# Optimization experiments

Hardware: AMD Instinct MI355X
Metric: run time of the kernel (lower is better)

Reference implementation:

```python
import jax, jax.numpy as jnp
import numpy as np

N = 27            # hardcoded node count in the module
D = 1024          # state_dim
E = D * 5         # MHA embed dim = 5120
H = 4             # n_heads


def setup_inputs() -> dict:
    key = jax.random.key(0)
    ks = jax.random.split(key, 6)
    s = 0.02
    return {
        "node_states": jax.random.normal(ks[0], (N, D, 5), jnp.float32),
        "hist_prev": jax.random.normal(ks[1], (N, D, 5), jnp.float32),
        "granger_w": jax.random.normal(ks[2], (1, 2 * E), jnp.float32) * s,
        "granger_b": jnp.zeros((1,), jnp.float32),
        "in_proj_w": jax.random.normal(ks[3], (3 * E, E), jnp.float32) * s,
        "in_proj_b": jnp.zeros((3 * E,), jnp.float32),
        "out_proj_w": jax.random.normal(ks[4], (E, E), jnp.float32) * s,
        "out_proj_b": jnp.zeros((E,), jnp.float32),
        "light_hertz": 500,
    }


def _mha(x, in_w, in_b, out_w, out_b):
    # x: [N, E]; torch MultiheadAttention with q=k=v=x, batch of 1
    qkv = x @ in_w.T + in_b                       # [N, 3E]
    q, k, v = jnp.split(qkv, 3, axis=-1)          # each [N, E]
    hd = E // H
    q = q.reshape(N, H, hd).transpose(1, 0, 2)    # [H, N, hd]
    k = k.reshape(N, H, hd).transpose(1, 0, 2)
    v = v.reshape(N, H, hd).transpose(1, 0, 2)
    scores = jnp.einsum('hqd,hkd->hqk', q, k) / jnp.sqrt(jnp.float32(hd))
    attn = jax.nn.softmax(scores, axis=-1)        # [H, N, N]
    o = jnp.einsum('hqk,hkd->hqd', attn, v)       # [H, N, hd]
    o = o.transpose(1, 0, 2).reshape(N, E)
    return o @ out_w.T + out_b                    # [N, E]


def reference(node_states, hist_prev, granger_w, granger_b,
              in_proj_w, in_proj_b, out_proj_w, out_proj_b, light_hertz):
    node_flat = node_states.reshape(N, E)         # [N, E]
    hist_flat = hist_prev.reshape(N, E)           # [N, E]

    # Granger pairwise test, vectorized: pred_input = [hist[j], node[i]]
    # score[i, j] = sigmoid(hist[j] . w_h + node[i] . w_n + b)
    w_h = granger_w[0, :E]
    w_n = granger_w[0, E:]
    col = node_flat @ w_n                          # [N] -> varies with i
    row = hist_flat @ w_h                          # [N] -> varies with j
    adj = jax.nn.sigmoid(col[:, None] + row[None, :] + granger_b[0])  # [N, N]
    causal_adj = adj * (1.0 - jnp.eye(N, dtype=adj.dtype))            # zero diagonal

    hertz_weight = jnp.clip(jnp.float32(light_hertz) / 1000.0, 0.1, 1.0)
    attended = _mha(node_flat, in_proj_w, in_proj_b, out_proj_w, out_proj_b)
    out = (attended * hertz_weight).reshape(N, D, 5)
    return out, causal_adj
```

## Files before the change

kernel.cpp:

```cpp
#include <hip/hip_runtime.h>

#define NROW 27
#define EDIM 5120
#define QKVDIM 15360
#define HD 1280

typedef __attribute__((ext_vector_type(8))) short bf16x8;
typedef __attribute__((ext_vector_type(4))) float f32x4;

__device__ inline short f2bf(float x) {
    unsigned u = __builtin_bit_cast(unsigned, x);
    u = (u + 0x7FFFu + ((u >> 16) & 1u)) >> 16;
    return (short)u;
}
__device__ inline float bf2f(short h) {
    unsigned u = ((unsigned)(unsigned short)h) << 16;
    return __builtin_bit_cast(float, u);
}

#define KC 64
#define LDK 72

__global__ __launch_bounds__(256)
void gemm_bf16x2(const float* __restrict__ X, const float* __restrict__ W,
                 float* __restrict__ Cp, int K, int Ntot, int Kblk)
{
    __shared__ short Whi[128][LDK];
    __shared__ short Wlo[128][LDK];
    __shared__ short Xhi[32][LDK];
    __shared__ short Xlo[32][LDK];

    const int tid = threadIdx.x;
    const int n0 = blockIdx.x * 128;
    const int k0 = blockIdx.y * Kblk;

    const int lane = tid & 63;
    const int wv   = tid >> 6;
    const int lm   = lane & 15;
    const int q8   = (lane >> 4) * 8;

    f32x4 acc[2][2] = {};

    const int wr  = tid >> 1;
    const int wkh = (tid & 1) * 32;
    const float* wp = W + (size_t)(n0 + wr) * K + k0 + wkh;

    const int xr = tid >> 3;
    const int xk = (tid & 7) * 8;
    const bool xok = (xr < NROW);
    const float* xp = X + (size_t)(xok ? xr : 0) * K + k0 + xk;

    for (int kc = 0; kc < Kblk; kc += KC) {
        float wbuf[32];
        #pragma unroll
        for (int i = 0; i < 8; ++i)
            *(float4*)&wbuf[4 * i] = ((const float4*)wp)[i];
        #pragma unroll
        for (int g = 0; g < 4; ++g) {
            bf16x8 h8, l8;
            #pragma unroll
            for (int j = 0; j < 8; ++j) {
                float f = wbuf[8 * g + j];
                short h = f2bf(f);
                h8[j] = h;
                l8[j] = f2bf(f - bf2f(h));
            }
            *(bf16x8*)&Whi[wr][wkh + 8 * g] = h8;
            *(bf16x8*)&Wlo[wr][wkh + 8 * g] = l8;
        }
        {
            float xbuf[8];
            if (xok) {
                *(float4*)&xbuf[0] = ((const float4*)xp)[0];
                *(float4*)&xbuf[4] = ((const float4*)xp)[1];
            } else {
                #pragma unroll
                for (int j = 0; j < 8; ++j) xbuf[j] = 0.f;
            }
            bf16x8 h8, l8;
            #pragma unroll
            for (int j = 0; j < 8; ++j) {
                short h = f2bf(xbuf[j]);
                h8[j] = h;
                l8[j] = f2bf(xbuf[j] - bf2f(h));
            }
            *(bf16x8*)&Xhi[xr][xk] = h8;
            *(bf16x8*)&Xlo[xr][xk] = l8;
        }
        __syncthreads();

        #pragma unroll
        for (int s = 0; s < 2; ++s) {
            const int ko = 32 * s + q8;
            bf16x8 ah0 = *(const bf16x8*)&Xhi[lm][ko];
            bf16x8 ah1 = *(const bf16x8*)&Xhi[lm + 16][ko];
            bf16x8 al0 = *(const bf16x8*)&Xlo[lm][ko];
            bf16x8 al1 = *(const bf16x8*)&Xlo[lm + 16][ko];
            bf16x8 bh0 = *(const bf16x8*)&Whi[32 * wv + lm][ko];
            bf16x8 bh1 = *(const bf16x8*)&Whi[32 * wv + 16 + lm][ko];
            bf16x8 bl0 = *(const bf16x8*)&Wlo[32 * wv + lm][ko];
            bf16x8 bl1 = *(const bf16x8*)&Wlo[32 * wv + 16 + lm][ko];

            acc[0][0] = __builtin_amdgcn_mfma_f32_16x16x32_bf16(ah0, bh0, acc[0][0], 0, 0, 0);
            acc[0][0] = __builtin_amdgcn_mfma_f32_16x16x32_bf16(ah0, bl0, acc[0][0], 0, 0, 0);
            acc[0][0] = __builtin_amdgcn_mfma_f32_16x16x32_bf16(al0, bh0, acc[0][0], 0, 0, 0);

            acc[0][1] = __builtin_amdgcn_mfma_f32_16x16x32_bf16(ah0, bh1, acc[0][1], 0, 0, 0);
            acc[0][1] = __builtin_amdgcn_mfma_f32_16x16x32_bf16(ah0, bl1, acc[0][1], 0, 0, 0);
            acc[0][1] = __builtin_amdgcn_mfma_f32_16x16x32_bf16(al0, bh1, acc[0][1], 0, 0, 0);

            acc[1][0] = __builtin_amdgcn_mfma_f32_16x16x32_bf16(ah1, bh0, acc[1][0], 0, 0, 0);
            acc[1][0] = __builtin_amdgcn_mfma_f32_16x16x32_bf16(ah1, bl0, acc[1][0], 0, 0, 0);
            acc[1][0] = __builtin_amdgcn_mfma_f32_16x16x32_bf16(al1, bh0, acc[1][0], 0, 0, 0);

            acc[1][1] = __builtin_amdgcn_mfma_f32_16x16x32_bf16(ah1, bh1, acc[1][1], 0, 0, 0);
            acc[1][1] = __builtin_amdgcn_mfma_f32_16x16x32_bf16(ah1, bl1, acc[1][1], 0, 0, 0);
            acc[1][1] = __builtin_amdgcn_mfma_f32_16x16x32_bf16(al1, bh1, acc[1][1], 0, 0, 0);
        }
        __syncthreads();
        wp += KC;
        xp += KC;
    }

    const size_t base = (size_t)blockIdx.y * NROW * Ntot;
    #pragma unroll
    for (int mi = 0; mi < 2; ++mi) {
        #pragma unroll
        for (int r = 0; r < 4; ++r) {
            const int m = mi * 16 + (lane >> 4) * 4 + r;
            if (m < NROW) {
                #pragma unroll
                for (int ni = 0; ni < 2; ++ni) {
                    const int n = n0 + 32 * wv + ni * 16 + lm;
                    Cp[base + (size_t)m * Ntot + n] = acc[mi][ni][r];
                }
            }
        }
    }
}

__global__ __launch_bounds__(256)
void reduce_kernel(const float* __restrict__ Cp, const float* __restrict__ bias,
                   float* __restrict__ out, int Ntot, int nky, const int* __restrict__ hz)
{
    const int idx = blockIdx.x * 256 + threadIdx.x;
    const int total4 = NROW * Ntot / 4;
    if (idx >= total4) return;
    float4 s = ((const float4*)Cp)[idx];
    for (int k = 1; k < nky; ++k) {
        float4 p = ((const float4*)(Cp + (size_t)k * NROW * Ntot))[idx];
        s.x += p.x; s.y += p.y; s.z += p.z; s.w += p.w;
    }
    const int n = (idx * 4) % Ntot;
    float4 b = *(const float4*)(bias + n);
    s.x += b.x; s.y += b.y; s.z += b.z; s.w += b.w;
    if (hz) {
        float h = (float)hz[0] * 0.001f;
        float sc = fminf(fmaxf(h, 0.1f), 1.0f);
        s.x *= sc; s.y *= sc; s.z *= sc; s.w *= sc;
    }
    ((float4*)out)[idx] = s;
}

__global__ __launch_bounds__(256)
void colrow_kernel(const float* __restrict__ node, const float* __restrict__ hist,
                   const float* __restrict__ gw, float* __restrict__ cr)
{
    const int b = blockIdx.x;
    const float* x = (b < NROW) ? node + (size_t)b * EDIM : hist + (size_t)(b - NROW) * EDIM;
    const float* w = (b < NROW) ? gw + EDIM : gw;
    const int tid = threadIdx.x;
    float a = 0.f;
    for (int f = tid; f < EDIM / 4; f += 256) {
        float4 xv = ((const float4*)x)[f];
        float4 wv = ((const float4*)w)[f];
        a += xv.x * wv.x + xv.y * wv.y + xv.z * wv.z + xv.w * wv.w;
    }
    #pragma unroll
    for (int off = 32; off; off >>= 1) a += __shfl_down(a, off);
    __shared__ float red[4];
    if ((tid & 63) == 0) red[tid >> 6] = a;
    __syncthreads();
    if (tid == 0) cr[b] = red[0] + red[1] + red[2] + red[3];
}

__global__ void adj_kernel(const float* __restrict__ cr, const float* __restrict__ gb,
                           float* __restrict__ adj)
{
    const int t = threadIdx.x;
    if (t < NROW * NROW) {
        const int i = t / NROW, j = t % NROW;
        float v = 0.f;
        if (i != j) {
            float z = cr[i] + cr[NROW + j] + gb[0];
            v = 1.0f / (1.0f + expf(-z));
        }
        adj[t] = v;
    }
}

__global__ __launch_bounds__(256)
void attn_kernel(const float* __restrict__ qkv, float* __restrict__ O)
{
    __shared__ float qs[HD];
    __shared__ float sc[NROW];
    __shared__ float pr[NROW];
    const int bx = blockIdx.x;
    const int h = bx & 3;
    const int i = bx >> 2;
    const int tid = threadIdx.x;

    const size_t qoff = (size_t)i * QKVDIM + (size_t)h * HD;
    for (int d = tid; d < HD; d += 256) qs[d] = qkv[qoff + d];
    __syncthreads();

    const int wid = tid >> 6, lane = tid & 63;
    for (int j = wid; j < NROW; j += 4) {
        const float* kr = qkv + (size_t)j * QKVDIM + EDIM + (size_t)h * HD;
        float a = 0.f;
        #pragma unroll
        for (int it = 0; it < 5; ++it) {
            int d4 = lane + 64 * it;
            float4 k4 = *(const float4*)(kr + 4 * d4);
            float4 q4 = *(const float4*)(qs + 4 * d4);
            a += q4.x * k4.x + q4.y * k4.y + q4.z * k4.z + q4.w * k4.w;
        }
        #pragma unroll
        for (int off = 32; off; off >>= 1) a += __shfl_down(a, off);
        if (lane == 0) sc[j] = a * 0.02795084971874737f;
    }
    __syncthreads();

    float mxv = -1e30f;
    for (int j = 0; j < NROW; ++j) mxv = fmaxf(mxv, sc[j]);
    float s = 0.f;
    for (int j = 0; j < NROW; ++j) s += expf(sc[j] - mxv);
    if (tid < NROW) pr[tid] = expf(sc[tid] - mxv) / s;
    __syncthreads();

    for (int d4 = tid; d4 < HD / 4; d4 += 256) {
        float4 o = make_float4(0.f, 0.f, 0.f, 0.f);
        for (int j = 0; j < NROW; ++j) {
            const float4 v4 = *(const float4*)(qkv + (size_t)j * QKVDIM + 2 * EDIM + (size_t)h * HD + 4 * d4);
            const float p = pr[j];
            o.x = fmaf(p, v4.x, o.x);
            o.y = fmaf(p, v4.y, o.y);
            o.z = fmaf(p, v4.z, o.z);
            o.w = fmaf(p, v4.w, o.w);
        }
        *(float4*)(O + (size_t)i * EDIM + (size_t)h * HD + 4 * d4) = o;
    }
}

extern "C" void kernel_launch(void* const* d_in, const int* in_sizes, int n_in,
                              void* d_out, int out_size, void* d_ws, size_t ws_size,
                              hipStream_t stream)
{
    const float* node = (const float*)d_in[0];
    const float* hist = (const float*)d_in[1];
    const float* gw   = (const float*)d_in[2];
    const float* gb   = (const float*)d_in[3];
    const float* inw  = (const float*)d_in[4];
    const float* inb  = (const float*)d_in[5];
    const float* outw = (const float*)d_in[6];
    const float* outb = (const float*)d_in[7];
    const int*   hz   = (const int*)d_in[8];

    float* out = (float*)d_out;

    float* Cp1  = (float*)d_ws;
    float* qkvf = Cp1 + (size_t)4 * NROW * QKVDIM;
    float* Obuf = qkvf + (size_t)NROW * QKVDIM;
    float* Cp2  = Obuf + (size_t)NROW * EDIM;
    float* cr   = Cp2 + (size_t)8 * NROW * EDIM;

    colrow_kernel<<<54, 256, 0, stream>>>(node, hist, gw, cr);
    adj_kernel<<<1, 768, 0, stream>>>(cr, gb, out + (size_t)NROW * EDIM);

    gemm_bf16x2<<<dim3(120, 4), 256, 0, stream>>>(node, inw, Cp1, EDIM, QKVDIM, EDIM / 4);
    reduce_kernel<<<(NROW * QKVDIM / 4 + 255) / 256, 256, 0, stream>>>(Cp1, inb, qkvf, QKVDIM, 4, nullptr);

    attn_kernel<<<108, 256, 0, stream>>>(qkvf, Obuf);

    gemm_bf16x2<<<dim3(40, 8), 256, 0, stream>>>(Obuf, outw, Cp2, EDIM, EDIM, EDIM / 8);
    reduce_kernel<<<(NROW * EDIM / 4 + 255) / 256, 256, 0, stream>>>(Cp2, outb, out, EDIM, 8, hz);
}
```

Measured before the change: 550.2 us.

## Prefetch next K-chunk in GEMM, double split-K, fuse adjacency into reduce

The GEMM now loads the next chunk of W and X from global memory into registers right after the shared-memory barrier, so the loads overlap the MFMA work on the current chunk. Split-K is doubled for both GEMMs (8 and 16 slices), which raises the block count to fill more CUs but enlarges the partial-sum workspace and the reduce traffic. The separate adjacency kernel is removed and its work runs in an extra final block of the last reduce kernel, saving one launch. The register prefetch raises register pressure and may lower occupancy.

After: 540.1 us. No clear change (-1.8%).

```diff
diff --git a/kernel.cpp b/kernel.cpp
--- a/kernel.cpp
+++ b/kernel.cpp
@@ -21,6 +21,21 @@
 #define KC 64
 #define LDK 72
 
+__device__ inline void loadW8(float* wbuf, const float* wp) {
+    #pragma unroll
+    for (int i = 0; i < 8; ++i)
+        *(float4*)&wbuf[4 * i] = ((const float4*)wp)[i];
+}
+__device__ inline void loadX2(float* xbuf, const float* xp, bool xok) {
+    if (xok) {
+        *(float4*)&xbuf[0] = ((const float4*)xp)[0];
+        *(float4*)&xbuf[4] = ((const float4*)xp)[1];
+    } else {
+        #pragma unroll
+        for (int j = 0; j < 8; ++j) xbuf[j] = 0.f;
+    }
+}
+
 __global__ __launch_bounds__(256)
 void gemm_bf16x2(const float* __restrict__ X, const float* __restrict__ W,
                  float* __restrict__ Cp, int K, int Ntot, int Kblk)
@@ -44,17 +59,16 @@
     const int wr  = tid >> 1;
     const int wkh = (tid & 1) * 32;
     const float* wp = W + (size_t)(n0 + wr) * K + k0 + wkh;
-
     const int xr = tid >> 3;
     const int xk = (tid & 7) * 8;
     const bool xok = (xr < NROW);
     const float* xp = X + (size_t)(xok ? xr : 0) * K + k0 + xk;
 
+    float wbuf[32], xbuf[8];
+    loadW8(wbuf, wp);
+    loadX2(xbuf, xp, xok);
+
     for (int kc = 0; kc < Kblk; kc += KC) {
-        float wbuf[32];
-        #pragma unroll
-        for (int i = 0; i < 8; ++i)
-            *(float4*)&wbuf[4 * i] = ((const float4*)wp)[i];
         #pragma unroll
         for (int g = 0; g < 4; ++g) {
             bf16x8 h8, l8;
@@ -69,14 +83,6 @@
             *(bf16x8*)&Wlo[wr][wkh + 8 * g] = l8;
         }
         {
-            float xbuf[8];
-            if (xok) {
-                *(float4*)&xbuf[0] = ((const float4*)xp)[0];
-                *(float4*)&xbuf[4] = ((const float4*)xp)[1];
-            } else {
-                #pragma unroll
-                for (int j = 0; j < 8; ++j) xbuf[j] = 0.f;
-            }
             bf16x8 h8, l8;
             #pragma unroll
             for (int j = 0; j < 8; ++j) {
@@ -88,6 +94,12 @@
             *(bf16x8*)&Xlo[xr][xk] = l8;
         }
         __syncthreads();
+
+        if (kc + KC < Kblk) {
+            wp += KC; xp += KC;
+            loadW8(wbuf, wp);
+            loadX2(xbuf, xp, xok);
+        }
 
         #pragma unroll
         for (int s = 0; s < 2; ++s) {
@@ -118,8 +130,6 @@
             acc[1][1] = __builtin_amdgcn_mfma_f32_16x16x32_bf16(al1, bh1, acc[1][1], 0, 0, 0);
         }
         __syncthreads();
-        wp += KC;
-        xp += KC;
     }
 
     const size_t base = (size_t)blockIdx.y * NROW * Ntot;
@@ -141,8 +151,22 @@
 
 __global__ __launch_bounds__(256)
 void reduce_kernel(const float* __restrict__ Cp, const float* __restrict__ bias,
-                   float* __restrict__ out, int Ntot, int nky, const int* __restrict__ hz)
-{
+                   float* __restrict__ out, int Ntot, int nky, const int* __restrict__ hz,
+                   const float* __restrict__ cr, const float* __restrict__ gb,
+                   float* __restrict__ adj)
+{
+    if (adj && blockIdx.x == gridDim.x - 1) {
+        for (int t = threadIdx.x; t < NROW * NROW; t += 256) {
+            const int i = t / NROW, j = t % NROW;
+            float v = 0.f;
+            if (i != j) {
+                float z = cr[i] + cr[NROW + j] + gb[0];
+                v = 1.0f / (1.0f + expf(-z));
+            }
+            adj[t] = v;
+        }
+        return;
+    }
     const int idx = blockIdx.x * 256 + threadIdx.x;
     const int total4 = NROW * Ntot / 4;
     if (idx >= total4) return;
@@ -184,21 +208,6 @@
     if (tid == 0) cr[b] = red[0] + red[1] + red[2] + red[3];
 }
 
-__global__ void adj_kernel(const float* __restrict__ cr, const float* __restrict__ gb,
-                           float* __restrict__ adj)
-{
-    const int t = threadIdx.x;
-    if (t < NROW * NROW) {
-        const int i = t / NROW, j = t % NROW;
-        float v = 0.f;
-        if (i != j) {
-            float z = cr[i] + cr[NROW + j] + gb[0];
-            v = 1.0f / (1.0f + expf(-z));
-        }
-        adj[t] = v;
-    }
-}
-
 __global__ __launch_bounds__(256)
 void attn_kernel(const float* __restrict__ qkv, float* __restrict__ O)
 {
@@ -269,19 +278,20 @@
     float* out = (float*)d_out;
 
     float* Cp1  = (float*)d_ws;
-    float* qkvf = Cp1 + (size_t)4 * NROW * QKVDIM;
+    float* qkvf = Cp1 + (size_t)8 * NROW * QKVDIM;
     float* Obuf = qkvf + (size_t)NROW * QKVDIM;
     float* Cp2  = Obuf + (size_t)NROW * EDIM;
-    float* cr   = Cp2 + (size_t)8 * NROW * EDIM;
+    float* cr   = Cp2 + (size_t)16 * NROW * EDIM;
 
     colrow_kernel<<<54, 256, 0, stream>>>(node, hist, gw, cr);
-    adj_kernel<<<1, 768, 0, stream>>>(cr, gb, out + (size_t)NROW * EDIM);
-
-    gemm_bf16x2<<<dim3(120, 4), 256, 0, stream>>>(node, inw, Cp1, EDIM, QKVDIM, EDIM / 4);
-    reduce_kernel<<<(NROW * QKVDIM / 4 + 255) / 256, 256, 0, stream>>>(Cp1, inb, qkvf, QKVDIM, 4, nullptr);
+
+    gemm_bf16x2<<<dim3(120, 8), 256, 0, stream>>>(node, inw, Cp1, EDIM, QKVDIM, EDIM / 8);
+    reduce_kernel<<<NROW * QKVDIM / 4 / 256, 256, 0, stream>>>(
+        Cp1, inb, qkvf, QKVDIM, 8, nullptr, nullptr, nullptr, nullptr);
 
     attn_kernel<<<108, 256, 0, stream>>>(qkvf, Obuf);
 
-    gemm_bf16x2<<<dim3(40, 8), 256, 0, stream>>>(Obuf, outw, Cp2, EDIM, EDIM, EDIM / 8);
-    reduce_kernel<<<(NROW * EDIM / 4 + 255) / 256, 256, 0, stream>>>(Cp2, outb, out, EDIM, 8, hz);
-}
+    gemm_bf16x2<<<dim3(40, 16), 256, 0, stream>>>(Obuf, outw, Cp2, EDIM, EDIM, EDIM / 16);
+    reduce_kernel<<<NROW * EDIM / 4 / 256 + 1, 256, 0, stream>>>(
+        Cp2, outb, out, EDIM, 16, hz, cr, gb, out + (size_t)NROW * EDIM);
+}
```
